# Kernel tuning notes

Measured on AMD Instinct MI355X. Metric: run time of the kernel, lower is better.

Reference implementation:

```python
import math
import jax, jax.numpy as jnp
import numpy as np

B, N, E, R = 1024, 200, 256, 256

def _layernorm(x, g, b, eps=1e-5):
    mu = x.mean(-1, keepdims=True)
    var = ((x - mu) ** 2).mean(-1, keepdims=True)
    return (x - mu) / jnp.sqrt(var + eps) * g + b

def setup_inputs() -> dict:
    key = jax.random.key(0)
    ks = jax.random.split(key, 16)
    d = {}
    d["e_emb"] = jax.random.normal(ks[0], (B, E), jnp.float32)
    d["nb_rel"] = jax.random.normal(ks[1], (B, N, R), jnp.float32)
    d["delta_t"] = jax.random.uniform(ks[2], (B, N), jnp.float32) * 10.0
    d["r_emb"] = jax.random.normal(ks[3], (B, R), jnp.float32)
    d["hist_mask"] = jax.random.randint(ks[4], (B, N), 0, 2).astype(bool)
    d["rel_w"] = jax.random.normal(ks[5], (E, R), jnp.float32) / math.sqrt(R)
    d["log_tau1"] = jnp.asarray(1.0, jnp.float32)
    d["log_tau2"] = jnp.asarray(2.5, jnp.float32)
    d["sharpness"] = jnp.asarray(1.5, jnp.float32)
    d["log_gamma"] = jnp.asarray(-2.0, jnp.float32)
    d["attn_w"] = jax.random.normal(ks[6], (3, E, E), jnp.float32) / math.sqrt(E)
    d["sp_w"] = jax.random.normal(ks[7], (3, E, 6 * E), jnp.float32) / math.sqrt(6 * E)
    d["sp_b"] = jnp.zeros((3, E), jnp.float32)
    d["ln_g"] = jnp.ones((3, E), jnp.float32)
    d["ln_b"] = jnp.zeros((3, E), jnp.float32)
    d["csq_w"] = jax.random.normal(ks[8], (E, R), jnp.float32) / math.sqrt(R)
    d["csq_b"] = jnp.zeros((E,), jnp.float32)
    d["csl_w"] = jax.random.normal(ks[9], (3, E), jnp.float32) / math.sqrt(E)
    d["csl_b"] = jnp.zeros((3,), jnp.float32)
    d["on_g"] = jnp.ones((E,), jnp.float32)
    d["on_b"] = jnp.zeros((E,), jnp.float32)
    return d

def _pna_one_scale(msgs, mask, e_emb, q_key, attn_w, sp_w, sp_b, ln_g, ln_b):
    # msgs: [B,N,E], mask: [B,N] bool, e_emb: [B,E], q_key: [B,E]
    valid_f = mask[..., None].astype(msgs.dtype)
    n_valid = jnp.maximum(mask.astype(msgs.dtype).sum(1, keepdims=True), 1.0)  # [B,1]
    msgs_v = msgs * valid_f
    mean_v = msgs_v.sum(1) / n_valid
    max_v = msgs_v.max(1)
    min_v = jnp.clip(jnp.where(mask[..., None], msgs, 10000.0).min(1), -10000.0, 10000.0)
    sq_m = (jnp.clip(msgs_v, -10.0, 10.0) ** 2).sum(1) / n_valid
    std_v = jnp.sqrt(jnp.maximum(sq_m - mean_v ** 2, 1e-6))
    q_proj = q_key @ attn_w.T  # [B,E]
    attn_raw = jnp.einsum('bne,be->bn', msgs, q_proj) / math.sqrt(msgs.shape[-1])
    attn_raw = jnp.where(mask, attn_raw, -10000.0)
    all_invalid = ~mask.any(1, keepdims=True)  # [B,1]
    attn_raw = jnp.where(all_invalid, 0.0, attn_raw)
    attn_p = jax.nn.softmax(attn_raw, axis=-1)
    attn_v = jnp.einsum('bn,bne->be', attn_p, msgs)
    feats = jnp.concatenate([mean_v, max_v, min_v, std_v, attn_v, e_emb], axis=-1)  # [B,6E]
    h = feats @ sp_w.T + sp_b
    h = _layernorm(h, ln_g, ln_b)
    return jax.nn.gelu(h, approximate=False)  # dropout = identity (eval mode)

def reference(e_emb, nb_rel, delta_t, r_emb, hist_mask, rel_w, log_tau1, log_tau2,
              sharpness, log_gamma, attn_w, sp_w, sp_b, ln_g, ln_b,
              csq_w, csq_b, csl_w, csl_b, on_g, on_b):
    msgs = jnp.einsum('bnr,er->bne', nb_rel, rel_w)
    gamma = jnp.exp(log_gamma)
    decay = jnp.exp(-gamma * jnp.maximum(delta_t, 0.0))
    msgs_dec = msgs * decay[..., None]
    tau1 = jnp.exp(log_tau1)
    tau2 = jnp.exp(log_tau2) + tau1
    sharp = jnp.clip(sharpness, 0.1, 5.0)
    w_fine = jax.nn.sigmoid(-sharp * (delta_t - tau1))
    w_coarse = jax.nn.sigmoid(sharp * (delta_t - tau2))
    w_mid = jnp.maximum(1.0 - w_fine - w_coarse, 0.0)
    scale_w = jnp.stack([w_fine, w_mid, w_coarse])  # [3,B,N]
    m_scales = msgs_dec[None] * scale_w[..., None]  # [3,B,N,E]
    q_key = r_emb @ rel_w.T  # [B,E]
    pna_v = jax.vmap(_pna_one_scale, in_axes=(0, None, None, None, 0, 0, 0, 0, 0))
    scales = pna_v(m_scales, hist_mask, e_emb, q_key, attn_w, sp_w, sp_b, ln_g, ln_b)  # [3,B,E]
    sq = r_emb @ csq_w.T + csq_b  # [B,E]
    logits = sq @ csl_w.T + csl_b  # [B,3]
    weights = jax.nn.softmax(logits, axis=-1)
    out = jnp.einsum('bs,sbe->be', weights, scales)
    return _layernorm(out, on_g, on_b)  # drop = identity (eval)
```

## Files before the change

kernel.cpp:

```cpp
#include <hip/hip_runtime.h>
#include <math.h>

#define B_   1024
#define N_   200
#define NR_  208
#define NT_  13
#define E_   256
#define R_   256
#define K6_  1536

typedef __attribute__((ext_vector_type(8))) short bf16x8;
typedef __attribute__((ext_vector_type(4))) float f32x4;

__device__ __forceinline__ unsigned short f2bf(float f) {
  unsigned int u = __float_as_uint(f);
  u += 0x7fffu + ((u >> 16) & 1u);
  return (unsigned short)(u >> 16);
}

__device__ __forceinline__ float gelu_exact(float x) {
  return 0.5f * x * (1.f + erff(x * 0.70710678118654752f));
}

__global__ __launch_bounds__(256) void k_cast(const float* __restrict__ rel_w,
                                              const float* __restrict__ sp_w,
                                              unsigned short* __restrict__ rw_bf,
                                              unsigned short* __restrict__ spw_bf) {
  int idx = blockIdx.x * 256 + threadIdx.x;
  if (idx < E_ * R_) rw_bf[idx] = f2bf(rel_w[idx]);
  int j = idx - E_ * R_;
  if (j >= 0 && j < 3 * E_ * K6_) spw_bf[j] = f2bf(sp_w[j]);
}

__global__ __launch_bounds__(256) void k_qkey(
    const float* __restrict__ r_emb, const float* __restrict__ rel_w,
    const float* __restrict__ csq_w, const float* __restrict__ csq_b,
    const float* __restrict__ csl_w, const float* __restrict__ csl_b,
    float* __restrict__ q_key, float* __restrict__ wts) {
  __shared__ __align__(16) float re[8][256];
  __shared__ __align__(16) float sqs[8][256];
  __shared__ float lg[8][3];
  int b0 = blockIdx.x * 8;
  int tid = threadIdx.x;
  for (int i = tid; i < 8 * 256; i += 256)
    re[i >> 8][i & 255] = r_emb[(size_t)(b0 + (i >> 8)) * 256 + (i & 255)];
  __syncthreads();
  int e = tid;
  float qk[8], sv[8];
#pragma unroll
  for (int i = 0; i < 8; ++i) { qk[i] = 0.f; sv[i] = 0.f; }
  const float4* w4 = (const float4*)(rel_w) + (size_t)e * 64;
  const float4* c4 = (const float4*)(csq_w) + (size_t)e * 64;
  for (int r = 0; r < 64; ++r) {
    float4 w = w4[r];
    float4 c = c4[r];
#pragma unroll
    for (int i = 0; i < 8; ++i) {
      float4 x = ((const float4*)re[i])[r];
      qk[i] += w.x * x.x + w.y * x.y + w.z * x.z + w.w * x.w;
      sv[i] += c.x * x.x + c.y * x.y + c.z * x.z + c.w * x.w;
    }
  }
  float cb = csq_b[e];
#pragma unroll
  for (int i = 0; i < 8; ++i) {
    q_key[(size_t)(b0 + i) * 256 + e] = qk[i];
    sqs[i][e] = sv[i] + cb;
  }
  __syncthreads();
  if (tid < 24) {
    int i = tid / 3, k = tid % 3;
    float acc = csl_b[k];
    for (int ee = 0; ee < 256; ++ee) acc += sqs[i][ee] * csl_w[k * 256 + ee];
    lg[i][k] = acc;
  }
  __syncthreads();
  if (tid < 8) {
    float l0 = lg[tid][0], l1 = lg[tid][1], l2 = lg[tid][2];
    float m = fmaxf(l0, fmaxf(l1, l2));
    float e0 = expf(l0 - m), e1 = expf(l1 - m), e2 = expf(l2 - m);
    float inv = 1.f / (e0 + e1 + e2);
    wts[(b0 + tid) * 4 + 0] = e0 * inv;
    wts[(b0 + tid) * 4 + 1] = e1 * inv;
    wts[(b0 + tid) * 4 + 2] = e2 * inv;
  }
}

__global__ __launch_bounds__(256) void k_qproj(const float* __restrict__ q_key,
                                               const float* __restrict__ attn_w,
                                               float* __restrict__ q_proj) {
  __shared__ __align__(16) float qk[8][256];
  int s = blockIdx.x >> 7;
  int b0 = (blockIdx.x & 127) * 8;
  int tid = threadIdx.x;
  for (int i = tid; i < 2048; i += 256)
    qk[i >> 8][i & 255] = q_key[(size_t)(b0 + (i >> 8)) * 256 + (i & 255)];
  __syncthreads();
  int e = tid;
  float acc[8];
#pragma unroll
  for (int i = 0; i < 8; ++i) acc[i] = 0.f;
  const float4* a4 = (const float4*)(attn_w) + ((size_t)s * 256 + e) * 64;
  for (int r = 0; r < 64; ++r) {
    float4 w = a4[r];
#pragma unroll
    for (int i = 0; i < 8; ++i) {
      float4 x = ((const float4*)qk[i])[r];
      acc[i] += w.x * x.x + w.y * x.y + w.z * x.z + w.w * x.w;
    }
  }
#pragma unroll
  for (int i = 0; i < 8; ++i)
    q_proj[((size_t)s * B_ + b0 + i) * 256 + e] = acc[i];
}

__global__ __launch_bounds__(256) void k_t(const float* __restrict__ q_proj,
                                           const float* __restrict__ rel_w,
                                           float* __restrict__ t_ws) {
  __shared__ __align__(16) float qp[8][256];
  int s = blockIdx.x >> 7;
  int b0 = (blockIdx.x & 127) * 8;
  int tid = threadIdx.x;
  for (int i = tid; i < 2048; i += 256)
    qp[i >> 8][i & 255] = q_proj[((size_t)s * B_ + b0 + (i >> 8)) * 256 + (i & 255)];
  __syncthreads();
  int r = tid;
  float acc[8];
#pragma unroll
  for (int i = 0; i < 8; ++i) acc[i] = 0.f;
  for (int e = 0; e < 256; ++e) {
    float w = rel_w[(size_t)e * 256 + r];
#pragma unroll
    for (int i = 0; i < 8; ++i) acc[i] = fmaf(qp[i][e], w, acc[i]);
  }
#pragma unroll
  for (int i = 0; i < 8; ++i)
    t_ws[((size_t)s * B_ + b0 + i) * 256 + r] = acc[i];
}

__global__ __launch_bounds__(512, 2) void k1_main(
    const float* __restrict__ nb_rel, const float* __restrict__ delta_t,
    const unsigned char* __restrict__ hm_raw, const float* __restrict__ e_emb,
    const float* __restrict__ p_lt1, const float* __restrict__ p_lt2,
    const float* __restrict__ p_sh, const float* __restrict__ p_lgm,
    const unsigned short* __restrict__ rw_bf, const float* __restrict__ t_ws,
    unsigned short* __restrict__ feats) {
  __shared__ __align__(16) struct {
    unsigned int a[NR_ * 132];
    float araw[3][NR_];
    float c[3][NR_];
    float p[3][NR_];
    float nmeta[NR_][9];
  } sm;
  int b = blockIdx.x;
  int tid = threadIdx.x;
  int lane = tid & 63, wave = tid >> 6;
  int row16 = lane & 15, quad = lane >> 4;

  float4 tf0 = *(const float4*)&t_ws[((size_t)0 * B_ + b) * 256 + lane * 4];
  float4 tf1 = *(const float4*)&t_ws[((size_t)1 * B_ + b) * 256 + lane * 4];
  float4 tf2 = *(const float4*)&t_ws[((size_t)2 * B_ + b) * 256 + lane * 4];

  int hasNZoff = 0, hasFP = 0;
  {
    unsigned char cc = hm_raw[tid];
    if ((tid & 3) != 0 && cc != 0) {
      hasNZoff = 1;
      if (cc == 0x3Fu || cc == 0x80u) hasFP = 1;
    }
  }
  int cntNZ = __syncthreads_count(hasNZoff);
  int cntFP = __syncthreads_count(hasFP);
  int mmode = (cntNZ == 0) ? 0 : (cntFP > 0 ? 2 : 1);

  float tau1 = expf(p_lt1[0]);
  float tau2 = expf(p_lt2[0]) + tau1;
  float sharp = fminf(fmaxf(p_sh[0], 0.1f), 5.0f);
  float gamma = expf(p_lgm[0]);

  bool mk = false;
  if (tid < NR_) {
    float mf = 0.f, c0 = 0.f, c1 = 0.f, c2 = 0.f;
    if (tid < N_) {
      size_t mi = (size_t)b * N_ + tid;
      if (mmode == 0)      mk = ((const int*)hm_raw)[mi] != 0;
      else if (mmode == 1) mk = hm_raw[mi] != 0;
      else                 mk = ((const float*)hm_raw)[mi] != 0.f;
      float dt = delta_t[mi];
      mf = mk ? 1.f : 0.f;
      float decay = expf(-gamma * fmaxf(dt, 0.f));
      float wf = 1.f / (1.f + expf(sharp * (dt - tau1)));
      float wc = 1.f / (1.f + expf(-sharp * (dt - tau2)));
      float wm = fmaxf(1.f - wf - wc, 0.f);
      c0 = decay * wf; c1 = decay * wm; c2 = decay * wc;
    }
    sm.c[0][tid] = c0; sm.c[1][tid] = c1; sm.c[2][tid] = c2;
    sm.nmeta[tid][0] = mf * c0;
    sm.nmeta[tid][1] = mf * c1;
    sm.nmeta[tid][2] = mf * c2;
    sm.nmeta[tid][3] = mk ? 0.f : 1e4f;
    sm.nmeta[tid][7] = mf;
  }
  int cnt = __syncthreads_count(mk ? 1 : 0);
  float nvf = fmaxf((float)cnt, 1.f);
  bool allinv = (cnt == 0);

  {
    const float* src = nb_rel + (size_t)b * N_ * 256;
    int n0 = wave;
    int g0 = (n0 < N_) ? n0 : (N_ - 1);
    float4 x = *(const float4*)(src + (size_t)g0 * 256 + lane * 4);
    for (int i = 0; i < 26; ++i) {
      int ncur = i * 8 + wave;
      float4 xn;
      if (i < 25) {
        int nn = (i + 1) * 8 + wave;
        int gn = (nn < N_) ? nn : (N_ - 1);
        xn = *(const float4*)(src + (size_t)gn * 256 + lane * 4);
      }
      float d0 = x.x * tf0.x + x.y * tf0.y + x.z * tf0.z + x.w * tf0.w;
      float d1 = x.x * tf1.x + x.y * tf1.y + x.z * tf1.z + x.w * tf1.w;
      float d2 = x.x * tf2.x + x.y * tf2.y + x.z * tf2.z + x.w * tf2.w;
#pragma unroll
      for (int o = 1; o < 64; o <<= 1) {
        d0 += __shfl_xor(d0, o, 64);
        d1 += __shfl_xor(d1, o, 64);
        d2 += __shfl_xor(d2, o, 64);
      }
      if (lane < 3) sm.araw[lane][ncur] = (lane == 0) ? d0 : ((lane == 1) ? d1 : d2);
      uint2 pk;
      pk.x = (unsigned int)f2bf(x.x) | ((unsigned int)f2bf(x.y) << 16);
      pk.y = (unsigned int)f2bf(x.z) | ((unsigned int)f2bf(x.w) << 16);
      *(uint2*)&sm.a[ncur * 132 + lane * 2] = pk;
      x = xn;
    }
  }

  bf16x8 bfr[2][8];
#pragma unroll
  for (int t = 0; t < 2; ++t) {
    int e = wave * 32 + t * 16 + row16;
#pragma unroll
    for (int ks = 0; ks < 8; ++ks)
      bfr[t][ks] = *(const bf16x8*)(rw_bf + (size_t)e * 256 + ks * 32 + quad * 8);
  }
  __syncthreads();

  if (tid < NR_) {
    float l0 = -1e30f, l1 = -1e30f, l2 = -1e30f;
    if (tid < N_) {
      bool mkk = sm.nmeta[tid][7] > 0.5f;
      l0 = sm.c[0][tid] * sm.araw[0][tid] * 0.0625f;
      l1 = sm.c[1][tid] * sm.araw[1][tid] * 0.0625f;
      l2 = sm.c[2][tid] * sm.araw[2][tid] * 0.0625f;
      l0 = mkk ? l0 : -1e4f; l1 = mkk ? l1 : -1e4f; l2 = mkk ? l2 : -1e4f;
      if (allinv) { l0 = 0.f; l1 = 0.f; l2 = 0.f; }
    }
    sm.p[0][tid] = l0; sm.p[1][tid] = l1; sm.p[2][tid] = l2;
  }
  __syncthreads();

  if (wave < 3) {
    int s = wave;
    float m = -1e30f;
    for (int n = lane; n < NR_; n += 64) m = fmaxf(m, sm.p[s][n]);
#pragma unroll
    for (int o = 32; o >= 1; o >>= 1) m = fmaxf(m, __shfl_xor(m, o, 64));
    float ssum = 0.f;
    for (int n = lane; n < NR_; n += 64) ssum += expf(sm.p[s][n] - m);
#pragma unroll
    for (int o = 32; o >= 1; o >>= 1) ssum += __shfl_xor(ssum, o, 64);
    float inv = 1.f / ssum;
    for (int n = lane; n < NR_; n += 64) {
      float pv = expf(sm.p[s][n] - m) * inv;
      sm.nmeta[n][4 + s] = pv * sm.c[s][n];
    }
  } else if (wave == 3) {
    for (int i = lane; i < 256; i += 64) {
      unsigned short v = f2bf(e_emb[(size_t)b * 256 + i]);
      feats[((size_t)0 * B_ + b) * K6_ + 1280 + i] = v;
      feats[((size_t)1 * B_ + b) * K6_ + 1280 + i] = v;
      feats[((size_t)2 * B_ + b) * K6_ + 1280 + i] = v;
    }
  }
  __syncthreads();

  float s_mean[3][2], s_mx[3][2], s_mn[3][2], s_sq[3][2], s_av[3][2];
#pragma unroll
  for (int s = 0; s < 3; ++s)
#pragma unroll
    for (int t = 0; t < 2; ++t) {
      s_mean[s][t] = 0.f; s_mx[s][t] = -1e30f; s_mn[s][t] = 1e30f;
      s_sq[s][t] = 0.f; s_av[s][t] = 0.f;
    }

  for (int nt = 0; nt < NT_; ++nt) {
    f32x4 acc[2];
#pragma unroll
    for (int t = 0; t < 2; ++t)
#pragma unroll
      for (int cc = 0; cc < 4; ++cc) acc[t][cc] = 0.f;
#pragma unroll
    for (int ks = 0; ks < 8; ++ks) {
      bf16x8 af = *(const bf16x8*)&sm.a[(nt * 16 + row16) * 132 + ks * 16 + quad * 4];
      acc[0] = __builtin_amdgcn_mfma_f32_16x16x32_bf16(af, bfr[0][ks], acc[0], 0, 0, 0);
      acc[1] = __builtin_amdgcn_mfma_f32_16x16x32_bf16(af, bfr[1][ks], acc[1], 0, 0, 0);
    }
    int nb = nt * 16 + quad * 4;
#pragma unroll
    for (int rg = 0; rg < 4; ++rg) {
      int n = nb + rg;
      float cmv[3], qv[3];
      cmv[0] = sm.nmeta[n][0]; cmv[1] = sm.nmeta[n][1]; cmv[2] = sm.nmeta[n][2];
      float off = sm.nmeta[n][3];
      qv[0] = sm.nmeta[n][4]; qv[1] = sm.nmeta[n][5]; qv[2] = sm.nmeta[n][6];
#pragma unroll
      for (int t = 0; t < 2; ++t) {
        float m = acc[t][rg];
#pragma unroll
        for (int s = 0; s < 3; ++s) {
          float vm = cmv[s] * m;
          s_mean[s][t] += vm;
          s_mx[s][t] = fmaxf(s_mx[s][t], vm);
          float mnc = fmaf(cmv[s], m, off);
          s_mn[s][t] = fminf(s_mn[s][t], mnc);
          float cv = fminf(fmaxf(vm, -10.f), 10.f);
          s_sq[s][t] = fmaf(cv, cv, s_sq[s][t]);
          s_av[s][t] = fmaf(qv[s], m, s_av[s][t]);
        }
      }
    }
  }

#pragma unroll
  for (int s = 0; s < 3; ++s) {
#pragma unroll
    for (int t = 0; t < 2; ++t) {
      float vmean = s_mean[s][t];
      vmean += __shfl_xor(vmean, 16, 64); vmean += __shfl_xor(vmean, 32, 64);
      float vmx = s_mx[s][t];
      vmx = fmaxf(vmx, __shfl_xor(vmx, 16, 64)); vmx = fmaxf(vmx, __shfl_xor(vmx, 32, 64));
      float vmn = s_mn[s][t];
      vmn = fminf(vmn, __shfl_xor(vmn, 16, 64)); vmn = fminf(vmn, __shfl_xor(vmn, 32, 64));
      float vsq = s_sq[s][t];
      vsq += __shfl_xor(vsq, 16, 64); vsq += __shfl_xor(vsq, 32, 64);
      float vav = s_av[s][t];
      vav += __shfl_xor(vav, 16, 64); vav += __shfl_xor(vav, 32, 64);
      if (lane < 16) {
        int e = wave * 32 + t * 16 + lane;
        size_t base = ((size_t)s * B_ + b) * K6_;
        float meanv = vmean / nvf;
        float stdv = sqrtf(fmaxf(vsq / nvf - meanv * meanv, 1e-6f));
        float mnv = fminf(fmaxf(vmn, -1e4f), 1e4f);
        feats[base + e] = f2bf(meanv);
        feats[base + 256 + e] = f2bf(vmx);
        feats[base + 512 + e] = f2bf(mnv);
        feats[base + 768 + e] = f2bf(stdv);
        feats[base + 1024 + e] = f2bf(vav);
      }
    }
  }
}

__global__ __launch_bounds__(256) void k2_kernel(
    const unsigned short* __restrict__ feats, const unsigned short* __restrict__ spw_bf,
    const float* __restrict__ sp_b, const float* __restrict__ ln_g,
    const float* __restrict__ ln_b, float* __restrict__ scales) {
  __shared__ __align__(16) union {
    unsigned int a[32 * 132];
    float h[32 * 260];
  } sm;
  int s = blockIdx.x >> 5;
  int b0 = (blockIdx.x & 31) * 32;
  int tid = threadIdx.x, lane = tid & 63, wave = tid >> 6;
  int row16 = lane & 15, quad = lane >> 4;
  int ebase = wave * 64;
  f32x4 acc[2][4];
#pragma unroll
  for (int mt = 0; mt < 2; ++mt)
#pragma unroll
    for (int t = 0; t < 4; ++t)
#pragma unroll
      for (int cc = 0; cc < 4; ++cc) acc[mt][t][cc] = 0.f;

  for (int kc = 0; kc < 6; ++kc) {
    __syncthreads();
    for (int j = tid; j < 1024; j += 256) {
      int rw = j >> 5, ck = j & 31;
      bf16x8 v = *(const bf16x8*)(feats + ((size_t)s * B_ + b0 + rw) * K6_ + kc * 256 + ck * 8);
      *(bf16x8*)((unsigned short*)&sm.a[rw * 132] + ck * 8) = v;
    }
    __syncthreads();
#pragma unroll
    for (int ks = 0; ks < 8; ++ks) {
      bf16x8 bfr[4];
#pragma unroll
      for (int t = 0; t < 4; ++t) {
        int e = ebase + t * 16 + row16;
        int k = kc * 256 + ks * 32 + quad * 8;
        bfr[t] = *(const bf16x8*)(spw_bf + ((size_t)s * E_ + e) * K6_ + k);
      }
#pragma unroll
      for (int mt = 0; mt < 2; ++mt) {
        bf16x8 af = *(const bf16x8*)&sm.a[(mt * 16 + row16) * 132 + ks * 16 + quad * 4];
#pragma unroll
        for (int t = 0; t < 4; ++t)
          acc[mt][t] = __builtin_amdgcn_mfma_f32_16x16x32_bf16(af, bfr[t], acc[mt][t], 0, 0, 0);
      }
    }
  }
  __syncthreads();
#pragma unroll
  for (int mt = 0; mt < 2; ++mt)
#pragma unroll
    for (int t = 0; t < 4; ++t)
#pragma unroll
      for (int rg = 0; rg < 4; ++rg) {
        int rw = mt * 16 + quad * 4 + rg;
        int e = ebase + t * 16 + row16;
        sm.h[rw * 260 + e] = acc[mt][t][rg] + sp_b[s * 256 + e];
      }
  __syncthreads();
  for (int rr = 0; rr < 8; ++rr) {
    int rw = wave * 8 + rr;
    float4 x = *(const float4*)&sm.h[rw * 260 + lane * 4];
    float sum = x.x + x.y + x.z + x.w;
    float sq = x.x * x.x + x.y * x.y + x.z * x.z + x.w * x.w;
#pragma unroll
    for (int o = 32; o >= 1; o >>= 1) {
      sum += __shfl_xor(sum, o, 64);
      sq += __shfl_xor(sq, o, 64);
    }
    float mu = sum * (1.f / 256.f);
    float var = sq * (1.f / 256.f) - mu * mu;
    float rstd = rsqrtf(var + 1e-5f);
    float4 g = *(const float4*)(ln_g + s * 256 + lane * 4);
    float4 bb = *(const float4*)(ln_b + s * 256 + lane * 4);
    float4 o4;
    o4.x = gelu_exact((x.x - mu) * rstd * g.x + bb.x);
    o4.y = gelu_exact((x.y - mu) * rstd * g.y + bb.y);
    o4.z = gelu_exact((x.z - mu) * rstd * g.z + bb.z);
    o4.w = gelu_exact((x.w - mu) * rstd * g.w + bb.w);
    *(float4*)(scales + ((size_t)s * B_ + b0 + rw) * 256 + lane * 4) = o4;
  }
}

__global__ __launch_bounds__(256) void k3_kernel(
    const float* __restrict__ scales, const float* __restrict__ wts,
    const float* __restrict__ on_g, const float* __restrict__ on_b,
    float* __restrict__ out) {
  __shared__ float rs[4], rq[4];
  int b = blockIdx.x, tid = threadIdx.x, lane = tid & 63, wave = tid >> 6;
  float w0 = wts[b * 4 + 0], w1 = wts[b * 4 + 1], w2 = wts[b * 4 + 2];
  float o = w0 * scales[((size_t)0 * B_ + b) * 256 + tid] +
            w1 * scales[((size_t)1 * B_ + b) * 256 + tid] +
            w2 * scales[((size_t)2 * B_ + b) * 256 + tid];
  float sum = o, sq = o * o;
#pragma unroll
  for (int off = 32; off >= 1; off >>= 1) {
    sum += __shfl_xor(sum, off, 64);
    sq += __shfl_xor(sq, off, 64);
  }
  if (lane == 0) { rs[wave] = sum; rq[wave] = sq; }
  __syncthreads();
  float ts = rs[0] + rs[1] + rs[2] + rs[3];
  float tq = rq[0] + rq[1] + rq[2] + rq[3];
  float mu = ts * (1.f / 256.f);
  float var = tq * (1.f / 256.f) - mu * mu;
  float rstd = rsqrtf(var + 1e-5f);
  out[(size_t)b * 256 + tid] = (o - mu) * rstd * on_g[tid] + on_b[tid];
}

extern "C" void kernel_launch(void* const* d_in, const int* in_sizes, int n_in,
                              void* d_out, int out_size, void* d_ws, size_t ws_size,
                              hipStream_t stream) {
  const float* e_emb   = (const float*)d_in[0];
  const float* nb_rel  = (const float*)d_in[1];
  const float* delta_t = (const float*)d_in[2];
  const float* r_emb   = (const float*)d_in[3];
  const unsigned char* hist_mask = (const unsigned char*)d_in[4];
  const float* rel_w   = (const float*)d_in[5];
  const float* lt1     = (const float*)d_in[6];
  const float* lt2     = (const float*)d_in[7];
  const float* shp     = (const float*)d_in[8];
  const float* lgm     = (const float*)d_in[9];
  const float* attn_w  = (const float*)d_in[10];
  const float* sp_w    = (const float*)d_in[11];
  const float* sp_b    = (const float*)d_in[12];
  const float* ln_g    = (const float*)d_in[13];
  const float* ln_b    = (const float*)d_in[14];
  const float* csq_w   = (const float*)d_in[15];
  const float* csq_b   = (const float*)d_in[16];
  const float* csl_w   = (const float*)d_in[17];
  const float* csl_b   = (const float*)d_in[18];
  const float* on_g    = (const float*)d_in[19];
  const float* on_b    = (const float*)d_in[20];
  float* out = (float*)d_out;

  char* ws = (char*)d_ws;
  unsigned short* rw_bf  = (unsigned short*)(ws + 0);
  unsigned short* spw_bf = (unsigned short*)(ws + 131072);
  float* q_key  = (float*)(ws + 2490368);
  float* q_proj = (float*)(ws + 3538944);
  float* t_ws   = (float*)(ws + 6684672);
  float* wts    = (float*)(ws + 9830400);
  unsigned short* feats = (unsigned short*)(ws + 9846784);
  float* scales = (float*)(ws + 19283968);

  hipLaunchKernelGGL(k_cast, dim3(4864), dim3(256), 0, stream, rel_w, sp_w, rw_bf, spw_bf);
  hipLaunchKernelGGL(k_qkey, dim3(128), dim3(256), 0, stream, r_emb, rel_w, csq_w, csq_b,
                     csl_w, csl_b, q_key, wts);
  hipLaunchKernelGGL(k_qproj, dim3(384), dim3(256), 0, stream, q_key, attn_w, q_proj);
  hipLaunchKernelGGL(k_t, dim3(384), dim3(256), 0, stream, q_proj, rel_w, t_ws);
  hipLaunchKernelGGL(k1_main, dim3(1024), dim3(512), 0, stream, nb_rel, delta_t, hist_mask,
                     e_emb, lt1, lt2, shp, lgm, rw_bf, t_ws, feats);
  hipLaunchKernelGGL(k2_kernel, dim3(96), dim3(256), 0, stream, feats, spw_bf, sp_b,
                     ln_g, ln_b, scales);
  hipLaunchKernelGGL(k3_kernel, dim3(1024), dim3(256), 0, stream, scales, wts, on_g, on_b, out);
}
```

Baseline: 537.8 us.

## Fuse query-projection prep kernels, widen k1 blocks, split k2 GEMM finer, move LN+GELU into k3

Merges the three small prep kernels (q_key/weights, q_proj, t) into one kernel working on 4 batch rows per block, so q_key and q_proj are no longer written to and read back from global memory. k1_main now runs 1024 threads per block, each wave owning 16 output columns instead of 32, which lowers per-thread register and accumulator use. The sp GEMM in k2 is split into 384 blocks of 16 rows by 128 columns, up from 96 blocks, to fill more compute units. The per-scale LayerNorm and GELU move from k2 into k3, which adds extra block reductions and syncs in k3 and a float intermediate buffer.

```diff
diff --git a/kernel.cpp b/kernel.cpp
--- a/kernel.cpp
+++ b/kernel.cpp
@@ -32,50 +32,56 @@
   if (j >= 0 && j < 3 * E_ * K6_) spw_bf[j] = f2bf(sp_w[j]);
 }
 
-__global__ __launch_bounds__(256) void k_qkey(
+__global__ __launch_bounds__(256) void k_prep(
     const float* __restrict__ r_emb, const float* __restrict__ rel_w,
     const float* __restrict__ csq_w, const float* __restrict__ csq_b,
     const float* __restrict__ csl_w, const float* __restrict__ csl_b,
-    float* __restrict__ q_key, float* __restrict__ wts) {
-  __shared__ __align__(16) float re[8][256];
-  __shared__ __align__(16) float sqs[8][256];
-  __shared__ float lg[8][3];
-  int b0 = blockIdx.x * 8;
+    const float* __restrict__ attn_w,
+    float* __restrict__ t_ws, float* __restrict__ wts) {
+  __shared__ __align__(16) float re[4][256];
+  __shared__ __align__(16) float qk[4][256];
+  __shared__ __align__(16) float sqs[4][256];
+  __shared__ __align__(16) float qp[3][4][256];
+  __shared__ float lg[4][3];
+  int b0 = blockIdx.x * 4;
   int tid = threadIdx.x;
-  for (int i = tid; i < 8 * 256; i += 256)
-    re[i >> 8][i & 255] = r_emb[(size_t)(b0 + (i >> 8)) * 256 + (i & 255)];
-  __syncthreads();
   int e = tid;
-  float qk[8], sv[8];
-#pragma unroll
-  for (int i = 0; i < 8; ++i) { qk[i] = 0.f; sv[i] = 0.f; }
-  const float4* w4 = (const float4*)(rel_w) + (size_t)e * 64;
-  const float4* c4 = (const float4*)(csq_w) + (size_t)e * 64;
-  for (int r = 0; r < 64; ++r) {
-    float4 w = w4[r];
-    float4 c = c4[r];
-#pragma unroll
-    for (int i = 0; i < 8; ++i) {
-      float4 x = ((const float4*)re[i])[r];
-      qk[i] += w.x * x.x + w.y * x.y + w.z * x.z + w.w * x.w;
-      sv[i] += c.x * x.x + c.y * x.y + c.z * x.z + c.w * x.w;
-    }
-  }
-  float cb = csq_b[e];
-#pragma unroll
-  for (int i = 0; i < 8; ++i) {
-    q_key[(size_t)(b0 + i) * 256 + e] = qk[i];
-    sqs[i][e] = sv[i] + cb;
-  }
-  __syncthreads();
-  if (tid < 24) {
+#pragma unroll
+  for (int i = 0; i < 4; ++i)
+    re[i][tid] = r_emb[(size_t)(b0 + i) * 256 + tid];
+  __syncthreads();
+  {
+    float qkv[4], sv[4];
+#pragma unroll
+    for (int i = 0; i < 4; ++i) { qkv[i] = 0.f; sv[i] = 0.f; }
+    const float4* w4 = (const float4*)(rel_w) + (size_t)e * 64;
+    const float4* c4 = (const float4*)(csq_w) + (size_t)e * 64;
+    for (int r = 0; r < 64; ++r) {
+      float4 w = w4[r];
+      float4 c = c4[r];
+#pragma unroll
+      for (int i = 0; i < 4; ++i) {
+        float4 x = ((const float4*)re[i])[r];
+        qkv[i] += w.x * x.x + w.y * x.y + w.z * x.z + w.w * x.w;
+        sv[i] += c.x * x.x + c.y * x.y + c.z * x.z + c.w * x.w;
+      }
+    }
+    float cb = csq_b[e];
+#pragma unroll
+    for (int i = 0; i < 4; ++i) {
+      qk[i][e] = qkv[i];
+      sqs[i][e] = sv[i] + cb;
+    }
+  }
+  __syncthreads();
+  if (tid < 12) {
     int i = tid / 3, k = tid % 3;
     float acc = csl_b[k];
     for (int ee = 0; ee < 256; ++ee) acc += sqs[i][ee] * csl_w[k * 256 + ee];
     lg[i][k] = acc;
   }
   __syncthreads();
-  if (tid < 8) {
+  if (tid < 4) {
     float l0 = lg[tid][0], l1 = lg[tid][1], l2 = lg[tid][2];
     float m = fmaxf(l0, fmaxf(l1, l2));
     float e0 = expf(l0 - m), e1 = expf(l1 - m), e2 = expf(l2 - m);
@@ -84,61 +90,67 @@
     wts[(b0 + tid) * 4 + 1] = e1 * inv;
     wts[(b0 + tid) * 4 + 2] = e2 * inv;
   }
-}
-
-__global__ __launch_bounds__(256) void k_qproj(const float* __restrict__ q_key,
-                                               const float* __restrict__ attn_w,
-                                               float* __restrict__ q_proj) {
-  __shared__ __align__(16) float qk[8][256];
-  int s = blockIdx.x >> 7;
-  int b0 = (blockIdx.x & 127) * 8;
-  int tid = threadIdx.x;
-  for (int i = tid; i < 2048; i += 256)
-    qk[i >> 8][i & 255] = q_key[(size_t)(b0 + (i >> 8)) * 256 + (i & 255)];
-  __syncthreads();
-  int e = tid;
-  float acc[8];
-#pragma unroll
-  for (int i = 0; i < 8; ++i) acc[i] = 0.f;
-  const float4* a4 = (const float4*)(attn_w) + ((size_t)s * 256 + e) * 64;
-  for (int r = 0; r < 64; ++r) {
-    float4 w = a4[r];
-#pragma unroll
-    for (int i = 0; i < 8; ++i) {
-      float4 x = ((const float4*)qk[i])[r];
-      acc[i] += w.x * x.x + w.y * x.y + w.z * x.z + w.w * x.w;
-    }
-  }
-#pragma unroll
-  for (int i = 0; i < 8; ++i)
-    q_proj[((size_t)s * B_ + b0 + i) * 256 + e] = acc[i];
-}
-
-__global__ __launch_bounds__(256) void k_t(const float* __restrict__ q_proj,
-                                           const float* __restrict__ rel_w,
-                                           float* __restrict__ t_ws) {
-  __shared__ __align__(16) float qp[8][256];
-  int s = blockIdx.x >> 7;
-  int b0 = (blockIdx.x & 127) * 8;
-  int tid = threadIdx.x;
-  for (int i = tid; i < 2048; i += 256)
-    qp[i >> 8][i & 255] = q_proj[((size_t)s * B_ + b0 + (i >> 8)) * 256 + (i & 255)];
-  __syncthreads();
-  int r = tid;
-  float acc[8];
-#pragma unroll
-  for (int i = 0; i < 8; ++i) acc[i] = 0.f;
-  for (int e = 0; e < 256; ++e) {
-    float w = rel_w[(size_t)e * 256 + r];
-#pragma unroll
-    for (int i = 0; i < 8; ++i) acc[i] = fmaf(qp[i][e], w, acc[i]);
-  }
-#pragma unroll
-  for (int i = 0; i < 8; ++i)
-    t_ws[((size_t)s * B_ + b0 + i) * 256 + r] = acc[i];
-}
-
-__global__ __launch_bounds__(512, 2) void k1_main(
+  {
+    float qpv[3][4];
+#pragma unroll
+    for (int s = 0; s < 3; ++s)
+#pragma unroll
+      for (int i = 0; i < 4; ++i) qpv[s][i] = 0.f;
+#pragma unroll
+    for (int s = 0; s < 3; ++s) {
+      const float4* a4 = (const float4*)(attn_w) + ((size_t)s * 256 + e) * 64;
+      for (int r = 0; r < 64; ++r) {
+        float4 w = a4[r];
+#pragma unroll
+        for (int i = 0; i < 4; ++i) {
+          float4 x = ((const float4*)qk[i])[r];
+          qpv[s][i] += w.x * x.x + w.y * x.y + w.z * x.z + w.w * x.w;
+        }
+      }
+    }
+    __syncthreads();
+#pragma unroll
+    for (int s = 0; s < 3; ++s)
+#pragma unroll
+      for (int i = 0; i < 4; ++i) qp[s][i][e] = qpv[s][i];
+  }
+  __syncthreads();
+  {
+    int r = tid;
+    float tacc[3][4];
+#pragma unroll
+    for (int s = 0; s < 3; ++s)
+#pragma unroll
+      for (int i = 0; i < 4; ++i) tacc[s][i] = 0.f;
+    for (int e4 = 0; e4 < 64; ++e4) {
+      float4 qv[3][4];
+#pragma unroll
+      for (int s = 0; s < 3; ++s)
+#pragma unroll
+        for (int i = 0; i < 4; ++i)
+          qv[s][i] = ((const float4*)qp[s][i])[e4];
+#pragma unroll
+      for (int j = 0; j < 4; ++j) {
+        float w = rel_w[(size_t)(e4 * 4 + j) * 256 + r];
+#pragma unroll
+        for (int s = 0; s < 3; ++s)
+#pragma unroll
+          for (int i = 0; i < 4; ++i) {
+            float q = (j == 0) ? qv[s][i].x : (j == 1) ? qv[s][i].y
+                      : (j == 2) ? qv[s][i].z : qv[s][i].w;
+            tacc[s][i] = fmaf(q, w, tacc[s][i]);
+          }
+      }
+    }
+#pragma unroll
+    for (int s = 0; s < 3; ++s)
+#pragma unroll
+      for (int i = 0; i < 4; ++i)
+        t_ws[((size_t)s * B_ + b0 + i) * 256 + r] = tacc[s][i];
+  }
+}
+
+__global__ __launch_bounds__(1024, 4) void k1_main(
     const float* __restrict__ nb_rel, const float* __restrict__ delta_t,
     const unsigned char* __restrict__ hm_raw, const float* __restrict__ e_emb,
     const float* __restrict__ p_lt1, const float* __restrict__ p_lt2,
@@ -207,14 +219,12 @@
 
   {
     const float* src = nb_rel + (size_t)b * N_ * 256;
-    int n0 = wave;
-    int g0 = (n0 < N_) ? n0 : (N_ - 1);
-    float4 x = *(const float4*)(src + (size_t)g0 * 256 + lane * 4);
-    for (int i = 0; i < 26; ++i) {
-      int ncur = i * 8 + wave;
+    float4 x = *(const float4*)(src + (size_t)wave * 256 + lane * 4);
+    for (int i = 0; i < NT_; ++i) {
+      int ncur = i * 16 + wave;
       float4 xn;
-      if (i < 25) {
-        int nn = (i + 1) * 8 + wave;
+      if (i < NT_ - 1) {
+        int nn = (i + 1) * 16 + wave;
         int gn = (nn < N_) ? nn : (N_ - 1);
         xn = *(const float4*)(src + (size_t)gn * 256 + lane * 4);
       }
@@ -236,13 +246,12 @@
     }
   }
 
-  bf16x8 bfr[2][8];
-#pragma unroll
-  for (int t = 0; t < 2; ++t) {
-    int e = wave * 32 + t * 16 + row16;
+  bf16x8 bfr[8];
+  {
+    int e = wave * 16 + row16;
 #pragma unroll
     for (int ks = 0; ks < 8; ++ks)
-      bfr[t][ks] = *(const bf16x8*)(rw_bf + (size_t)e * 256 + ks * 32 + quad * 8);
+      bfr[ks] = *(const bf16x8*)(rw_bf + (size_t)e * 256 + ks * 32 + quad * 8);
   }
   __syncthreads();
 
@@ -285,176 +294,148 @@
   }
   __syncthreads();
 
-  float s_mean[3][2], s_mx[3][2], s_mn[3][2], s_sq[3][2], s_av[3][2];
-#pragma unroll
-  for (int s = 0; s < 3; ++s)
-#pragma unroll
-    for (int t = 0; t < 2; ++t) {
-      s_mean[s][t] = 0.f; s_mx[s][t] = -1e30f; s_mn[s][t] = 1e30f;
-      s_sq[s][t] = 0.f; s_av[s][t] = 0.f;
-    }
+  float s_mean[3], s_mx[3], s_mn[3], s_sq[3], s_av[3];
+#pragma unroll
+  for (int s = 0; s < 3; ++s) {
+    s_mean[s] = 0.f; s_mx[s] = -1e30f; s_mn[s] = 1e30f;
+    s_sq[s] = 0.f; s_av[s] = 0.f;
+  }
 
   for (int nt = 0; nt < NT_; ++nt) {
-    f32x4 acc[2];
-#pragma unroll
-    for (int t = 0; t < 2; ++t)
-#pragma unroll
-      for (int cc = 0; cc < 4; ++cc) acc[t][cc] = 0.f;
+    f32x4 acc;
+#pragma unroll
+    for (int cc = 0; cc < 4; ++cc) acc[cc] = 0.f;
 #pragma unroll
     for (int ks = 0; ks < 8; ++ks) {
       bf16x8 af = *(const bf16x8*)&sm.a[(nt * 16 + row16) * 132 + ks * 16 + quad * 4];
-      acc[0] = __builtin_amdgcn_mfma_f32_16x16x32_bf16(af, bfr[0][ks], acc[0], 0, 0, 0);
-      acc[1] = __builtin_amdgcn_mfma_f32_16x16x32_bf16(af, bfr[1][ks], acc[1], 0, 0, 0);
+      acc = __builtin_amdgcn_mfma_f32_16x16x32_bf16(af, bfr[ks], acc, 0, 0, 0);
     }
     int nb = nt * 16 + quad * 4;
 #pragma unroll
     for (int rg = 0; rg < 4; ++rg) {
       int n = nb + rg;
-      float cmv[3], qv[3];
-      cmv[0] = sm.nmeta[n][0]; cmv[1] = sm.nmeta[n][1]; cmv[2] = sm.nmeta[n][2];
+      float cm0 = sm.nmeta[n][0], cm1 = sm.nmeta[n][1], cm2 = sm.nmeta[n][2];
       float off = sm.nmeta[n][3];
-      qv[0] = sm.nmeta[n][4]; qv[1] = sm.nmeta[n][5]; qv[2] = sm.nmeta[n][6];
-#pragma unroll
-      for (int t = 0; t < 2; ++t) {
-        float m = acc[t][rg];
-#pragma unroll
-        for (int s = 0; s < 3; ++s) {
-          float vm = cmv[s] * m;
-          s_mean[s][t] += vm;
-          s_mx[s][t] = fmaxf(s_mx[s][t], vm);
-          float mnc = fmaf(cmv[s], m, off);
-          s_mn[s][t] = fminf(s_mn[s][t], mnc);
-          float cv = fminf(fmaxf(vm, -10.f), 10.f);
-          s_sq[s][t] = fmaf(cv, cv, s_sq[s][t]);
-          s_av[s][t] = fmaf(qv[s], m, s_av[s][t]);
-        }
+      float q0 = sm.nmeta[n][4], q1 = sm.nmeta[n][5], q2 = sm.nmeta[n][6];
+      float m = acc[rg];
+      float cmv[3] = {cm0, cm1, cm2};
+      float qv[3] = {q0, q1, q2};
+#pragma unroll
+      for (int s = 0; s < 3; ++s) {
+        float vm = cmv[s] * m;
+        s_mean[s] += vm;
+        s_mx[s] = fmaxf(s_mx[s], vm);
+        s_mn[s] = fminf(s_mn[s], fmaf(cmv[s], m, off));
+        float cv = fminf(fmaxf(vm, -10.f), 10.f);
+        s_sq[s] = fmaf(cv, cv, s_sq[s]);
+        s_av[s] = fmaf(qv[s], m, s_av[s]);
       }
     }
   }
 
 #pragma unroll
   for (int s = 0; s < 3; ++s) {
-#pragma unroll
-    for (int t = 0; t < 2; ++t) {
-      float vmean = s_mean[s][t];
-      vmean += __shfl_xor(vmean, 16, 64); vmean += __shfl_xor(vmean, 32, 64);
-      float vmx = s_mx[s][t];
-      vmx = fmaxf(vmx, __shfl_xor(vmx, 16, 64)); vmx = fmaxf(vmx, __shfl_xor(vmx, 32, 64));
-      float vmn = s_mn[s][t];
-      vmn = fminf(vmn, __shfl_xor(vmn, 16, 64)); vmn = fminf(vmn, __shfl_xor(vmn, 32, 64));
-      float vsq = s_sq[s][t];
-      vsq += __shfl_xor(vsq, 16, 64); vsq += __shfl_xor(vsq, 32, 64);
-      float vav = s_av[s][t];
-      vav += __shfl_xor(vav, 16, 64); vav += __shfl_xor(vav, 32, 64);
-      if (lane < 16) {
-        int e = wave * 32 + t * 16 + lane;
-        size_t base = ((size_t)s * B_ + b) * K6_;
-        float meanv = vmean / nvf;
-        float stdv = sqrtf(fmaxf(vsq / nvf - meanv * meanv, 1e-6f));
-        float mnv = fminf(fmaxf(vmn, -1e4f), 1e4f);
-        feats[base + e] = f2bf(meanv);
-        feats[base + 256 + e] = f2bf(vmx);
-        feats[base + 512 + e] = f2bf(mnv);
-        feats[base + 768 + e] = f2bf(stdv);
-        feats[base + 1024 + e] = f2bf(vav);
-      }
+    float vmean = s_mean[s];
+    vmean += __shfl_xor(vmean, 16, 64); vmean += __shfl_xor(vmean, 32, 64);
+    float vmx = s_mx[s];
+    vmx = fmaxf(vmx, __shfl_xor(vmx, 16, 64)); vmx = fmaxf(vmx, __shfl_xor(vmx, 32, 64));
+    float vmn = s_mn[s];
+    vmn = fminf(vmn, __shfl_xor(vmn, 16, 64)); vmn = fminf(vmn, __shfl_xor(vmn, 32, 64));
+    float vsq = s_sq[s];
+    vsq += __shfl_xor(vsq, 16, 64); vsq += __shfl_xor(vsq, 32, 64);
+    float vav = s_av[s];
+    vav += __shfl_xor(vav, 16, 64); vav += __shfl_xor(vav, 32, 64);
+    if (lane < 16) {
+      int e = wave * 16 + lane;
+      size_t base = ((size_t)s * B_ + b) * K6_;
+      float meanv = vmean / nvf;
+      float stdv = sqrtf(fmaxf(vsq / nvf - meanv * meanv, 1e-6f));
+      float mnv = fminf(fmaxf(vmn, -1e4f), 1e4f);
+      feats[base + e] = f2bf(meanv);
+      feats[base + 256 + e] = f2bf(vmx);
+      feats[base + 512 + e] = f2bf(mnv);
+      feats[base + 768 + e] = f2bf(stdv);
+      feats[base + 1024 + e] = f2bf(vav);
     }
   }
 }
 
 __global__ __launch_bounds__(256) void k2_kernel(
     const unsigned short* __restrict__ feats, const unsigned short* __restrict__ spw_bf,
-    const float* __restrict__ sp_b, const float* __restrict__ ln_g,
-    const float* __restrict__ ln_b, float* __restrict__ scales) {
-  __shared__ __align__(16) union {
-    unsigned int a[32 * 132];
-    float h[32 * 260];
-  } sm;
-  int s = blockIdx.x >> 5;
-  int b0 = (blockIdx.x & 31) * 32;
+    const float* __restrict__ sp_b, float* __restrict__ hbuf) {
+  __shared__ __align__(16) unsigned int a[16 * 132];
+  int id = blockIdx.x;
+  int s = id >> 7;
+  int rem = id & 127;
+  int b0 = (rem >> 1) * 16;
+  int e0 = (rem & 1) * 128;
   int tid = threadIdx.x, lane = tid & 63, wave = tid >> 6;
   int row16 = lane & 15, quad = lane >> 4;
-  int ebase = wave * 64;
-  f32x4 acc[2][4];
-#pragma unroll
-  for (int mt = 0; mt < 2; ++mt)
-#pragma unroll
-    for (int t = 0; t < 4; ++t)
-#pragma unroll
-      for (int cc = 0; cc < 4; ++cc) acc[mt][t][cc] = 0.f;
+  f32x4 acc[2];
+#pragma unroll
+  for (int t = 0; t < 2; ++t)
+#pragma unroll
+    for (int cc = 0; cc < 4; ++cc) acc[t][cc] = 0.f;
 
   for (int kc = 0; kc < 6; ++kc) {
     __syncthreads();
-    for (int j = tid; j < 1024; j += 256) {
+    for (int j = tid; j < 512; j += 256) {
       int rw = j >> 5, ck = j & 31;
       bf16x8 v = *(const bf16x8*)(feats + ((size_t)s * B_ + b0 + rw) * K6_ + kc * 256 + ck * 8);
-      *(bf16x8*)((unsigned short*)&sm.a[rw * 132] + ck * 8) = v;
+      *(bf16x8*)((unsigned short*)&a[rw * 132] + ck * 8) = v;
     }
     __syncthreads();
 #pragma unroll
     for (int ks = 0; ks < 8; ++ks) {
-      bf16x8 bfr[4];
-#pragma unroll
-      for (int t = 0; t < 4; ++t) {
-        int e = ebase + t * 16 + row16;
-        int k = kc * 256 + ks * 32 + quad * 8;
-        bfr[t] = *(const bf16x8*)(spw_bf + ((size_t)s * E_ + e) * K6_ + k);
-      }
-#pragma unroll
-      for (int mt = 0; mt < 2; ++mt) {
-        bf16x8 af = *(const bf16x8*)&sm.a[(mt * 16 + row16) * 132 + ks * 16 + quad * 4];
-#pragma unroll
-        for (int t = 0; t < 4; ++t)
-          acc[mt][t] = __builtin_amdgcn_mfma_f32_16x16x32_bf16(af, bfr[t], acc[mt][t], 0, 0, 0);
-      }
-    }
-  }
-  __syncthreads();
-#pragma unroll
-  for (int mt = 0; mt < 2; ++mt)
-#pragma unroll
-    for (int t = 0; t < 4; ++t)
-#pragma unroll
-      for (int rg = 0; rg < 4; ++rg) {
-        int rw = mt * 16 + quad * 4 + rg;
-        int e = ebase + t * 16 + row16;
-        sm.h[rw * 260 + e] = acc[mt][t][rg] + sp_b[s * 256 + e];
-      }
-  __syncthreads();
-  for (int rr = 0; rr < 8; ++rr) {
-    int rw = wave * 8 + rr;
-    float4 x = *(const float4*)&sm.h[rw * 260 + lane * 4];
-    float sum = x.x + x.y + x.z + x.w;
-    float sq = x.x * x.x + x.y * x.y + x.z * x.z + x.w * x.w;
-#pragma unroll
-    for (int o = 32; o >= 1; o >>= 1) {
-      sum += __shfl_xor(sum, o, 64);
-      sq += __shfl_xor(sq, o, 64);
-    }
-    float mu = sum * (1.f / 256.f);
-    float var = sq * (1.f / 256.f) - mu * mu;
-    float rstd = rsqrtf(var + 1e-5f);
-    float4 g = *(const float4*)(ln_g + s * 256 + lane * 4);
-    float4 bb = *(const float4*)(ln_b + s * 256 + lane * 4);
-    float4 o4;
-    o4.x = gelu_exact((x.x - mu) * rstd * g.x + bb.x);
-    o4.y = gelu_exact((x.y - mu) * rstd * g.y + bb.y);
-    o4.z = gelu_exact((x.z - mu) * rstd * g.z + bb.z);
-    o4.w = gelu_exact((x.w - mu) * rstd * g.w + bb.w);
-    *(float4*)(scales + ((size_t)s * B_ + b0 + rw) * 256 + lane * 4) = o4;
+      bf16x8 af = *(const bf16x8*)&a[row16 * 132 + ks * 16 + quad * 4];
+#pragma unroll
+      for (int t = 0; t < 2; ++t) {
+        int e = e0 + wave * 32 + t * 16 + row16;
+        bf16x8 bfr = *(const bf16x8*)(spw_bf + ((size_t)s * E_ + e) * K6_ + kc * 256 + ks * 32 + quad * 8);
+        acc[t] = __builtin_amdgcn_mfma_f32_16x16x32_bf16(af, bfr, acc[t], 0, 0, 0);
+      }
+    }
+  }
+#pragma unroll
+  for (int t = 0; t < 2; ++t) {
+    int e = e0 + wave * 32 + t * 16 + row16;
+    float bias = sp_b[s * 256 + e];
+#pragma unroll
+    for (int rg = 0; rg < 4; ++rg) {
+      int rw = quad * 4 + rg;
+      hbuf[((size_t)s * B_ + b0 + rw) * 256 + e] = acc[t][rg] + bias;
+    }
   }
 }
 
 __global__ __launch_bounds__(256) void k3_kernel(
-    const float* __restrict__ scales, const float* __restrict__ wts,
+    const float* __restrict__ hbuf, const float* __restrict__ wts,
+    const float* __restrict__ ln_g, const float* __restrict__ ln_b,
     const float* __restrict__ on_g, const float* __restrict__ on_b,
     float* __restrict__ out) {
   __shared__ float rs[4], rq[4];
   int b = blockIdx.x, tid = threadIdx.x, lane = tid & 63, wave = tid >> 6;
-  float w0 = wts[b * 4 + 0], w1 = wts[b * 4 + 1], w2 = wts[b * 4 + 2];
-  float o = w0 * scales[((size_t)0 * B_ + b) * 256 + tid] +
-            w1 * scales[((size_t)1 * B_ + b) * 256 + tid] +
-            w2 * scales[((size_t)2 * B_ + b) * 256 + tid];
+  float o = 0.f;
+#pragma unroll
+  for (int s = 0; s < 3; ++s) {
+    float h = hbuf[((size_t)s * B_ + b) * 256 + tid];
+    float sum = h, sq = h * h;
+#pragma unroll
+    for (int off = 32; off >= 1; off >>= 1) {
+      sum += __shfl_xor(sum, off, 64);
+      sq += __shfl_xor(sq, off, 64);
+    }
+    if (lane == 0) { rs[wave] = sum; rq[wave] = sq; }
+    __syncthreads();
+    float ts = rs[0] + rs[1] + rs[2] + rs[3];
+    float tq = rq[0] + rq[1] + rq[2] + rq[3];
+    __syncthreads();
+    float mu = ts * (1.f / 256.f);
+    float var = tq * (1.f / 256.f) - mu * mu;
+    float rstd = rsqrtf(var + 1e-5f);
+    float v = (h - mu) * rstd * ln_g[s * 256 + tid] + ln_b[s * 256 + tid];
+    o += wts[b * 4 + s] * gelu_exact(v);
+  }
   float sum = o, sq = o * o;
 #pragma unroll
   for (int off = 32; off >= 1; off >>= 1) {
@@ -500,21 +481,17 @@
   char* ws = (char*)d_ws;
   unsigned short* rw_bf  = (unsigned short*)(ws + 0);
   unsigned short* spw_bf = (unsigned short*)(ws + 131072);
-  float* q_key  = (float*)(ws + 2490368);
-  float* q_proj = (float*)(ws + 3538944);
-  float* t_ws   = (float*)(ws + 6684672);
-  float* wts    = (float*)(ws + 9830400);
-  unsigned short* feats = (unsigned short*)(ws + 9846784);
-  float* scales = (float*)(ws + 19283968);
+  float* t_ws   = (float*)(ws + 2490368);
+  float* wts    = (float*)(ws + 5636096);
+  unsigned short* feats = (unsigned short*)(ws + 5652480);
+  float* hbuf   = (float*)(ws + 15089664);
 
   hipLaunchKernelGGL(k_cast, dim3(4864), dim3(256), 0, stream, rel_w, sp_w, rw_bf, spw_bf);
-  hipLaunchKernelGGL(k_qkey, dim3(128), dim3(256), 0, stream, r_emb, rel_w, csq_w, csq_b,
-                     csl_w, csl_b, q_key, wts);
-  hipLaunchKernelGGL(k_qproj, dim3(384), dim3(256), 0, stream, q_key, attn_w, q_proj);
-  hipLaunchKernelGGL(k_t, dim3(384), dim3(256), 0, stream, q_proj, rel_w, t_ws);
-  hipLaunchKernelGGL(k1_main, dim3(1024), dim3(512), 0, stream, nb_rel, delta_t, hist_mask,
+  hipLaunchKernelGGL(k_prep, dim3(256), dim3(256), 0, stream, r_emb, rel_w, csq_w, csq_b,
+                     csl_w, csl_b, attn_w, t_ws, wts);
+  hipLaunchKernelGGL(k1_main, dim3(1024), dim3(1024), 0, stream, nb_rel, delta_t, hist_mask,
                      e_emb, lt1, lt2, shp, lgm, rw_bf, t_ws, feats);
-  hipLaunchKernelGGL(k2_kernel, dim3(96), dim3(256), 0, stream, feats, spw_bf, sp_b,
-                     ln_g, ln_b, scales);
-  hipLaunchKernelGGL(k3_kernel, dim3(1024), dim3(256), 0, stream, scales, wts, on_g, on_b, out);
-}
+  hipLaunchKernelGGL(k2_kernel, dim3(384), dim3(256), 0, stream, feats, spw_bf, sp_b, hbuf);
+  hipLaunchKernelGGL(k3_kernel, dim3(1024), dim3(256), 0, stream, hbuf, wts, ln_g, ln_b,
+                     on_g, on_b, out);
+}
```

Result: faster. 526.9 us (-2.0%).
